# Performance work log

Hardware: AMD Instinct MI355X
Metric: run time of the kernel (lower is better)

Reference implementation:

```python
import jax, jax.numpy as jnp
import numpy as np

D_MODEL = 1024
NUM_HEADS = 16
HEAD_DIM = D_MODEL // NUM_HEADS
B, S = 2, 2048


def setup_inputs() -> dict:
    key = jax.random.key(0)
    ks = jax.random.split(key, 5)
    x = jax.random.normal(ks[0], (B, S, D_MODEL), dtype=jnp.float32)
    # nn.Linear weights are [out_features, in_features]
    Wq = jax.random.normal(ks[1], (D_MODEL, D_MODEL), dtype=jnp.float32) / np.sqrt(D_MODEL)
    Wk = jax.random.normal(ks[2], (HEAD_DIM, D_MODEL), dtype=jnp.float32) / np.sqrt(D_MODEL)
    Wv = jax.random.normal(ks[3], (HEAD_DIM, D_MODEL), dtype=jnp.float32) / np.sqrt(D_MODEL)
    Wo = jax.random.normal(ks[4], (D_MODEL, D_MODEL), dtype=jnp.float32) / np.sqrt(D_MODEL)
    # causal mask, broadcastable to [B, H, S, S]; mask==0 positions get -inf
    mask = jnp.tril(jnp.ones((S, S), dtype=bool))[None, None]
    return {"x": x, "Wq": Wq, "Wk": Wk, "Wv": Wv, "Wo": Wo, "mask": mask}


def reference(x, Wq, Wk, Wv, Wo, mask):
    Bsz, Sl, D = x.shape
    H, hd = NUM_HEADS, HEAD_DIM
    q = (x @ Wq.T).reshape(Bsz, Sl, H, hd)          # [B,S,H,hd]
    k = x @ Wk.T                                    # [B,S,hd] (single shared KV head)
    v = x @ Wv.T                                    # [B,S,hd]
    scale = 1.0 / np.sqrt(hd).astype(np.float32)
    # scores: [B,H,S,S] — full O(n^2) matrix, as in the original module
    scores = jnp.einsum('bshd,btd->bhst', q, k) * scale
    scores = jnp.where(mask, scores, -jnp.inf)
    attn = jax.nn.softmax(scores, axis=-1)
    out = jnp.einsum('bhst,btd->bshd', attn, v).reshape(Bsz, Sl, D)
    return out @ Wo.T
```

## Files before the change

### kernel.cpp

```cpp
#include <hip/hip_runtime.h>
#include <hip/hip_bf16.h>
#include <math.h>

#define BB 2
#define SS 2048
#define DD 1024
#define NH 16
#define HD 64
#define MM (BB * SS)

#define BK 32

typedef __hip_bfloat16 bf16;
typedef __bf16 bf16_t;
typedef __attribute__((ext_vector_type(8))) __bf16 bf16x8;
typedef __attribute__((ext_vector_type(4))) __bf16 bf16x4;
typedef __attribute__((ext_vector_type(4))) float floatx4;

#define SCALEQ 0.18033688011112042f

__global__ void detect_dtype(const unsigned int* __restrict__ x, int* __restrict__ flag) {
    const int tid = threadIdx.x;
    int good = 0;
    for (int i = tid; i < 256; i += 64) {
        unsigned int bits = (x[i] & 0xFFFFu) << 16;
        float v = __uint_as_float(bits);
        float av = fabsf(v);
        if (av == 0.f || (av >= 9.5367431640625e-7f && av <= 64.f)) good++;
    }
#pragma unroll
    for (int s = 1; s < 64; s <<= 1) good += __shfl_xor(good, s);
    if (tid == 0) { flag[0] = (good >= 240) ? 0 : 1; flag[1] = 0; }
}

__device__ __forceinline__ void conv_seg(const void* __restrict__ in,
                                         bf16_t* __restrict__ out,
                                         int n, int f, int tid, int T) {
    if (f) {
        const float* p = (const float*)in;
        for (int i = tid * 8; i < n; i += T * 8) {
            float4 a = *(const float4*)(p + i);
            float4 b = *(const float4*)(p + i + 4);
            bf16x8 o;
            o[0] = (bf16_t)a.x; o[1] = (bf16_t)a.y; o[2] = (bf16_t)a.z; o[3] = (bf16_t)a.w;
            o[4] = (bf16_t)b.x; o[5] = (bf16_t)b.y; o[6] = (bf16_t)b.z; o[7] = (bf16_t)b.w;
            *(bf16x8*)(out + i) = o;
        }
    } else {
        const bf16_t* p = (const bf16_t*)in;
        for (int i = tid * 8; i < n; i += T * 8)
            *(bf16x8*)(out + i) = *(const bf16x8*)(p + i);
    }
}

__global__ __launch_bounds__(256) void conv_all(const void* __restrict__ x,
                                                const void* __restrict__ wq,
                                                const void* __restrict__ wk,
                                                const void* __restrict__ wv,
                                                const void* __restrict__ wo,
                                                bf16_t* __restrict__ xb,
                                                bf16_t* __restrict__ wqb,
                                                bf16_t* __restrict__ wkb,
                                                bf16_t* __restrict__ wvb,
                                                bf16_t* __restrict__ wob,
                                                const int* __restrict__ flag) {
    const int f = *flag;
    const int tid = blockIdx.x * blockDim.x + threadIdx.x;
    const int T = gridDim.x * blockDim.x;
    conv_seg(x, xb, MM * DD, f, tid, T);
    conv_seg(wq, wqb, DD * DD, f, tid, T);
    conv_seg(wk, wkb, HD * DD, f, tid, T);
    conv_seg(wv, wvb, HD * DD, f, tid, T);
    conv_seg(wo, wob, DD * DD, f, tid, T);
}

#define KP 40

__global__ __launch_bounds__(256) void proj_qkv_b(const bf16_t* __restrict__ X,
                                                  const bf16_t* __restrict__ Wq,
                                                  const bf16_t* __restrict__ Wk,
                                                  const bf16_t* __restrict__ Wv,
                                                  bf16_t* __restrict__ QA,
                                                  bf16_t* __restrict__ Kp,
                                                  bf16_t* __restrict__ VpT) {
    __shared__ bf16_t As[64 * KP];
    __shared__ bf16_t Bs[64 * KP];

    const int tid = threadIdx.x;
    const int wave = tid >> 6, lane = tid & 63;
    const int lo = lane & 15, quad = lane >> 4;
    const int wr = wave >> 1, wc = wave & 1;
    const int rowBase = blockIdx.x * 64;
    const int cb = blockIdx.y;

    const int rS = tid >> 2;
    const int c8 = (tid & 3) * 8;

    const bf16_t* arow = X + (size_t)(rowBase + rS) * DD + c8;
    const bf16_t* wrow;
    if (cb < 16)       wrow = Wq + (size_t)(cb * 64 + rS) * DD + c8;
    else if (cb == 16) wrow = Wk + (size_t)rS * DD + c8;
    else               wrow = Wv + (size_t)rS * DD + c8;

    floatx4 acc[2][2];
#pragma unroll
    for (int i = 0; i < 2; i++)
#pragma unroll
        for (int j = 0; j < 2; j++) acc[i][j] = (floatx4){0.f, 0.f, 0.f, 0.f};

    bf16x8 aR0 = *(const bf16x8*)(arow);
    bf16x8 bR0 = *(const bf16x8*)(wrow);
    bf16x8 aR1 = *(const bf16x8*)(arow + BK);
    bf16x8 bR1 = *(const bf16x8*)(wrow + BK);

    for (int k0 = 0; k0 < DD; k0 += 2 * BK) {
        __syncthreads();
        *(bf16x8*)&As[rS * KP + c8] = aR0;
        *(bf16x8*)&Bs[rS * KP + c8] = bR0;
        __syncthreads();
        if (k0 + 2 * BK < DD) {
            aR0 = *(const bf16x8*)(arow + k0 + 2 * BK);
            bR0 = *(const bf16x8*)(wrow + k0 + 2 * BK);
        }
        {
            bf16x8 afr[2], bfr[2];
#pragma unroll
            for (int i = 0; i < 2; i++)
                afr[i] = *(const bf16x8*)&As[(wr * 32 + i * 16 + lo) * KP + quad * 8];
#pragma unroll
            for (int j = 0; j < 2; j++)
                bfr[j] = *(const bf16x8*)&Bs[(wc * 32 + j * 16 + lo) * KP + quad * 8];
#pragma unroll
            for (int i = 0; i < 2; i++)
#pragma unroll
                for (int j = 0; j < 2; j++)
                    acc[i][j] = __builtin_amdgcn_mfma_f32_16x16x32_bf16(afr[i], bfr[j], acc[i][j], 0, 0, 0);
        }
        __syncthreads();
        *(bf16x8*)&As[rS * KP + c8] = aR1;
        *(bf16x8*)&Bs[rS * KP + c8] = bR1;
        __syncthreads();
        if (k0 + 3 * BK < DD) {
            aR1 = *(const bf16x8*)(arow + k0 + 3 * BK);
            bR1 = *(const bf16x8*)(wrow + k0 + 3 * BK);
        }
        {
            bf16x8 afr[2], bfr[2];
#pragma unroll
            for (int i = 0; i < 2; i++)
                afr[i] = *(const bf16x8*)&As[(wr * 32 + i * 16 + lo) * KP + quad * 8];
#pragma unroll
            for (int j = 0; j < 2; j++)
                bfr[j] = *(const bf16x8*)&Bs[(wc * 32 + j * 16 + lo) * KP + quad * 8];
#pragma unroll
            for (int i = 0; i < 2; i++)
#pragma unroll
                for (int j = 0; j < 2; j++)
                    acc[i][j] = __builtin_amdgcn_mfma_f32_16x16x32_bf16(afr[i], bfr[j], acc[i][j], 0, 0, 0);
        }
    }

#pragma unroll
    for (int i = 0; i < 2; i++)
#pragma unroll
        for (int j = 0; j < 2; j++)
#pragma unroll
            for (int reg = 0; reg < 4; reg++) {
                int row = rowBase + wr * 32 + i * 16 + quad * 4 + reg;
                int c = wc * 32 + j * 16 + lo;
                float v = acc[i][j][reg];
                if (cb < 16) {
                    QA[(size_t)row * DD + cb * 64 + c] = (bf16_t)(v * SCALEQ);
                } else if (cb == 16) {
                    Kp[(size_t)row * HD + c] = (bf16_t)v;
                } else {
                    VpT[((size_t)(row >> 11) * HD + c) * SS + (row & (SS - 1))] = (bf16_t)v;
                }
            }
}

__global__ __launch_bounds__(256) void proj_o_b(const bf16_t* __restrict__ AO,
                                                const bf16_t* __restrict__ Wo,
                                                void* __restrict__ Cout,
                                                const int* __restrict__ flagOut) {
    const int fout = *flagOut;

    __shared__ bf16_t As[64 * KP];
    __shared__ bf16_t Bs[64 * KP];

    const int tid = threadIdx.x;
    const int wave = tid >> 6, lane = tid & 63;
    const int lo = lane & 15, quad = lane >> 4;
    const int wr = wave >> 1, wc = wave & 1;
    const int rowBase = blockIdx.x * 64;
    const int colBase = blockIdx.y * 64;

    const int rS = tid >> 2;
    const int c8 = (tid & 3) * 8;

    const bf16_t* arow = AO + (size_t)(rowBase + rS) * DD + c8;
    const bf16_t* wrow = Wo + (size_t)(colBase + rS) * DD + c8;

    floatx4 acc[2][2];
#pragma unroll
    for (int i = 0; i < 2; i++)
#pragma unroll
        for (int j = 0; j < 2; j++) acc[i][j] = (floatx4){0.f, 0.f, 0.f, 0.f};

    bf16x8 aR0 = *(const bf16x8*)(arow);
    bf16x8 bR0 = *(const bf16x8*)(wrow);
    bf16x8 aR1 = *(const bf16x8*)(arow + BK);
    bf16x8 bR1 = *(const bf16x8*)(wrow + BK);

    for (int k0 = 0; k0 < DD; k0 += 2 * BK) {
        __syncthreads();
        *(bf16x8*)&As[rS * KP + c8] = aR0;
        *(bf16x8*)&Bs[rS * KP + c8] = bR0;
        __syncthreads();
        if (k0 + 2 * BK < DD) {
            aR0 = *(const bf16x8*)(arow + k0 + 2 * BK);
            bR0 = *(const bf16x8*)(wrow + k0 + 2 * BK);
        }
        {
            bf16x8 afr[2], bfr[2];
#pragma unroll
            for (int i = 0; i < 2; i++)
                afr[i] = *(const bf16x8*)&As[(wr * 32 + i * 16 + lo) * KP + quad * 8];
#pragma unroll
            for (int j = 0; j < 2; j++)
                bfr[j] = *(const bf16x8*)&Bs[(wc * 32 + j * 16 + lo) * KP + quad * 8];
#pragma unroll
            for (int i = 0; i < 2; i++)
#pragma unroll
                for (int j = 0; j < 2; j++)
                    acc[i][j] = __builtin_amdgcn_mfma_f32_16x16x32_bf16(afr[i], bfr[j], acc[i][j], 0, 0, 0);
        }
        __syncthreads();
        *(bf16x8*)&As[rS * KP + c8] = aR1;
        *(bf16x8*)&Bs[rS * KP + c8] = bR1;
        __syncthreads();
        if (k0 + 3 * BK < DD) {
            aR1 = *(const bf16x8*)(arow + k0 + 3 * BK);
            bR1 = *(const bf16x8*)(wrow + k0 + 3 * BK);
        }
        {
            bf16x8 afr[2], bfr[2];
#pragma unroll
            for (int i = 0; i < 2; i++)
                afr[i] = *(const bf16x8*)&As[(wr * 32 + i * 16 + lo) * KP + quad * 8];
#pragma unroll
            for (int j = 0; j < 2; j++)
                bfr[j] = *(const bf16x8*)&Bs[(wc * 32 + j * 16 + lo) * KP + quad * 8];
#pragma unroll
            for (int i = 0; i < 2; i++)
#pragma unroll
                for (int j = 0; j < 2; j++)
                    acc[i][j] = __builtin_amdgcn_mfma_f32_16x16x32_bf16(afr[i], bfr[j], acc[i][j], 0, 0, 0);
        }
    }

#pragma unroll
    for (int i = 0; i < 2; i++)
#pragma unroll
        for (int j = 0; j < 2; j++)
#pragma unroll
            for (int reg = 0; reg < 4; reg++) {
                int row = rowBase + wr * 32 + i * 16 + quad * 4 + reg;
                int col = colBase + wc * 32 + j * 16 + lo;
                size_t idx = (size_t)row * DD + col;
                if (fout) ((float*)Cout)[idx] = acc[i][j][reg];
                else      ((bf16_t*)Cout)[idx] = (bf16_t)acc[i][j][reg];
            }
}

__device__ __forceinline__ bf16x4 cvt4(float4 v) {
    bf16x4 o;
    o[0] = (bf16_t)v.x; o[1] = (bf16_t)v.y; o[2] = (bf16_t)v.z; o[3] = (bf16_t)v.w;
    return o;
}

__global__ __launch_bounds__(256) void proj_qkv(const void* __restrict__ X,
                                                const void* __restrict__ Wq,
                                                const void* __restrict__ Wk,
                                                const void* __restrict__ Wv,
                                                bf16_t* __restrict__ QA,
                                                bf16_t* __restrict__ Kp,
                                                bf16_t* __restrict__ VpT,
                                                const int* __restrict__ flag) {
    const int f = *flag;

    __shared__ bf16_t As[128 * KP];
    __shared__ bf16_t Ws[64 * KP];

    const int tid = threadIdx.x;
    const int wave = tid >> 6, lane = tid & 63;
    const int lo = lane & 15, quad = lane >> 4;
    const int rb = wave * 32;
    const int cb = blockIdx.x;
    const int rowBase = blockIdx.y * 128;

    floatx4 acc[2][4];
#pragma unroll
    for (int i = 0; i < 2; i++)
#pragma unroll
        for (int j = 0; j < 4; j++) acc[i][j] = (floatx4){0.f, 0.f, 0.f, 0.f};

    if (f) {
        const int rA = tid >> 3, sg = tid & 7;
        const float* arow[4];
        const float* wrow[2];
#pragma unroll
        for (int p = 0; p < 4; p++)
            arow[p] = (const float*)X + (size_t)(rowBase + rA + 32 * p) * DD;
#pragma unroll
        for (int p = 0; p < 2; p++) {
            int row = rA + 32 * p;
            if (cb < 16)       wrow[p] = (const float*)Wq + (size_t)(cb * 64 + row) * DD;
            else if (cb == 16) wrow[p] = (const float*)Wk + (size_t)row * DD;
            else               wrow[p] = (const float*)Wv + (size_t)row * DD;
        }
        float4 aR[4], wR[2];
#pragma unroll
        for (int p = 0; p < 4; p++) aR[p] = *(const float4*)(arow[p] + sg * 4);
#pragma unroll
        for (int p = 0; p < 2; p++) wR[p] = *(const float4*)(wrow[p] + sg * 4);

        for (int k0 = 0; k0 < DD; k0 += BK) {
            __syncthreads();
#pragma unroll
            for (int p = 0; p < 4; p++)
                *(bf16x4*)&As[(rA + 32 * p) * KP + sg * 4] = cvt4(aR[p]);
#pragma unroll
            for (int p = 0; p < 2; p++)
                *(bf16x4*)&Ws[(rA + 32 * p) * KP + sg * 4] = cvt4(wR[p]);
            __syncthreads();
            if (k0 + BK < DD) {
#pragma unroll
                for (int p = 0; p < 4; p++) aR[p] = *(const float4*)(arow[p] + k0 + BK + sg * 4);
#pragma unroll
                for (int p = 0; p < 2; p++) wR[p] = *(const float4*)(wrow[p] + k0 + BK + sg * 4);
            }
            bf16x8 afr[2], bfr[4];
#pragma unroll
            for (int i = 0; i < 2; i++)
                afr[i] = *(const bf16x8*)&As[(rb + i * 16 + lo) * KP + quad * 8];
#pragma unroll
            for (int j = 0; j < 4; j++)
                bfr[j] = *(const bf16x8*)&Ws[(j * 16 + lo) * KP + quad * 8];
#pragma unroll
            for (int i = 0; i < 2; i++)
#pragma unroll
                for (int j = 0; j < 4; j++)
                    acc[i][j] = __builtin_amdgcn_mfma_f32_16x16x32_bf16(afr[i], bfr[j], acc[i][j], 0, 0, 0);
        }
    } else {
        const int rA = tid >> 2, sg = tid & 3;
        const bf16_t* arow[2];
        const bf16_t* wrow;
#pragma unroll
        for (int p = 0; p < 2; p++)
            arow[p] = (const bf16_t*)X + (size_t)(rowBase + rA + 64 * p) * DD;
        if (cb < 16)       wrow = (const bf16_t*)Wq + (size_t)(cb * 64 + rA) * DD;
        else if (cb == 16) wrow = (const bf16_t*)Wk + (size_t)rA * DD;
        else               wrow = (const bf16_t*)Wv + (size_t)rA * DD;
        bf16x8 aR[2], wR;
#pragma unroll
        for (int p = 0; p < 2; p++) aR[p] = *(const bf16x8*)(arow[p] + sg * 8);
        wR = *(const bf16x8*)(wrow + sg * 8);

        for (int k0 = 0; k0 < DD; k0 += BK) {
            __syncthreads();
#pragma unroll
            for (int p = 0; p < 2; p++)
                *(bf16x8*)&As[(rA + 64 * p) * KP + sg * 8] = aR[p];
            *(bf16x8*)&Ws[rA * KP + sg * 8] = wR;
            __syncthreads();
            if (k0 + BK < DD) {
#pragma unroll
                for (int p = 0; p < 2; p++) aR[p] = *(const bf16x8*)(arow[p] + k0 + BK + sg * 8);
                wR = *(const bf16x8*)(wrow + k0 + BK + sg * 8);
            }
            bf16x8 afr[2], bfr[4];
#pragma unroll
            for (int i = 0; i < 2; i++)
                afr[i] = *(const bf16x8*)&As[(rb + i * 16 + lo) * KP + quad * 8];
#pragma unroll
            for (int j = 0; j < 4; j++)
                bfr[j] = *(const bf16x8*)&Ws[(j * 16 + lo) * KP + quad * 8];
#pragma unroll
            for (int i = 0; i < 2; i++)
#pragma unroll
                for (int j = 0; j < 4; j++)
                    acc[i][j] = __builtin_amdgcn_mfma_f32_16x16x32_bf16(afr[i], bfr[j], acc[i][j], 0, 0, 0);
        }
    }

#pragma unroll
    for (int i = 0; i < 2; i++)
#pragma unroll
        for (int j = 0; j < 4; j++)
#pragma unroll
            for (int reg = 0; reg < 4; reg++) {
                int row = rowBase + rb + i * 16 + quad * 4 + reg;
                int col = j * 16 + lo;
                if (cb < 16) {
                    QA[(size_t)row * DD + cb * 64 + col] = (bf16_t)(acc[i][j][reg] * SCALEQ);
                } else if (cb == 16) {
                    Kp[(size_t)row * HD + col] = (bf16_t)acc[i][j][reg];
                } else {
                    VpT[((size_t)(row >> 11) * HD + col) * SS + (row & (SS - 1))] =
                        (bf16_t)acc[i][j][reg];
                }
            }
}

__global__ __launch_bounds__(256) void proj_o(const bf16_t* __restrict__ AO,
                                              const void* __restrict__ Wo,
                                              void* __restrict__ Cout,
                                              const int* __restrict__ flagW,
                                              const int* __restrict__ flagOut) {
    const int f = *flagW;
    const int fout = *flagOut;

    __shared__ bf16_t As[128 * KP];
    __shared__ bf16_t Ws[64 * KP];

    const int tid = threadIdx.x;
    const int wave = tid >> 6, lane = tid & 63;
    const int lo = lane & 15, quad = lane >> 4;
    const int rb = wave * 32;
    const int colBase = blockIdx.x * 64;
    const int rowBase = blockIdx.y * 128;

    floatx4 acc[2][4];
#pragma unroll
    for (int i = 0; i < 2; i++)
#pragma unroll
        for (int j = 0; j < 4; j++) acc[i][j] = (floatx4){0.f, 0.f, 0.f, 0.f};

    const int rA2 = tid >> 2, sgA = tid & 3;
    const bf16_t* arow[2] = {AO + (size_t)(rowBase + rA2) * DD,
                             AO + (size_t)(rowBase + rA2 + 64) * DD};
    bf16x8 aR[2];
#pragma unroll
    for (int p = 0; p < 2; p++) aR[p] = *(const bf16x8*)(arow[p] + sgA * 8);

    if (f) {
        const int rW = tid >> 3, sgW = tid & 7;
        const float* wrow[2];
#pragma unroll
        for (int p = 0; p < 2; p++)
            wrow[p] = (const float*)Wo + (size_t)(colBase + rW + 32 * p) * DD;
        float4 wR[2];
#pragma unroll
        for (int p = 0; p < 2; p++) wR[p] = *(const float4*)(wrow[p] + sgW * 4);

        for (int k0 = 0; k0 < DD; k0 += BK) {
            __syncthreads();
#pragma unroll
            for (int p = 0; p < 2; p++)
                *(bf16x8*)&As[(rA2 + 64 * p) * KP + sgA * 8] = aR[p];
#pragma unroll
            for (int p = 0; p < 2; p++)
                *(bf16x4*)&Ws[(rW + 32 * p) * KP + sgW * 4] = cvt4(wR[p]);
            __syncthreads();
            if (k0 + BK < DD) {
#pragma unroll
                for (int p = 0; p < 2; p++) aR[p] = *(const bf16x8*)(arow[p] + k0 + BK + sgA * 8);
#pragma unroll
                for (int p = 0; p < 2; p++) wR[p] = *(const float4*)(wrow[p] + k0 + BK + sgW * 4);
            }
            bf16x8 afr[2], bfr[4];
#pragma unroll
            for (int i = 0; i < 2; i++)
                afr[i] = *(const bf16x8*)&As[(rb + i * 16 + lo) * KP + quad * 8];
#pragma unroll
            for (int j = 0; j < 4; j++)
                bfr[j] = *(const bf16x8*)&Ws[(j * 16 + lo) * KP + quad * 8];
#pragma unroll
            for (int i = 0; i < 2; i++)
#pragma unroll
                for (int j = 0; j < 4; j++)
                    acc[i][j] = __builtin_amdgcn_mfma_f32_16x16x32_bf16(afr[i], bfr[j], acc[i][j], 0, 0, 0);
        }
    } else {
        const bf16_t* wrow = (const bf16_t*)Wo + (size_t)(colBase + rA2) * DD;
        bf16x8 wR = *(const bf16x8*)(wrow + sgA * 8);

        for (int k0 = 0; k0 < DD; k0 += BK) {
            __syncthreads();
#pragma unroll
            for (int p = 0; p < 2; p++)
                *(bf16x8*)&As[(rA2 + 64 * p) * KP + sgA * 8] = aR[p];
            *(bf16x8*)&Ws[rA2 * KP + sgA * 8] = wR;
            __syncthreads();
            if (k0 + BK < DD) {
#pragma unroll
                for (int p = 0; p < 2; p++) aR[p] = *(const bf16x8*)(arow[p] + k0 + BK + sgA * 8);
                wR = *(const bf16x8*)(wrow + k0 + BK + sgA * 8);
            }
            bf16x8 afr[2], bfr[4];
#pragma unroll
            for (int i = 0; i < 2; i++)
                afr[i] = *(const bf16x8*)&As[(rb + i * 16 + lo) * KP + quad * 8];
#pragma unroll
            for (int j = 0; j < 4; j++)
                bfr[j] = *(const bf16x8*)&Ws[(j * 16 + lo) * KP + quad * 8];
#pragma unroll
            for (int i = 0; i < 2; i++)
#pragma unroll
                for (int j = 0; j < 4; j++)
                    acc[i][j] = __builtin_amdgcn_mfma_f32_16x16x32_bf16(afr[i], bfr[j], acc[i][j], 0, 0, 0);
        }
    }

#pragma unroll
    for (int i = 0; i < 2; i++)
#pragma unroll
        for (int j = 0; j < 4; j++)
#pragma unroll
            for (int reg = 0; reg < 4; reg++) {
                int row = rowBase + rb + i * 16 + quad * 4 + reg;
                int col = colBase + j * 16 + lo;
                size_t idx = (size_t)row * DD + col;
                if (fout) ((float*)Cout)[idx] = acc[i][j][reg];
                else      ((bf16_t*)Cout)[idx] = (bf16_t)acc[i][j][reg];
            }
}

#define PSTR 40
#define DMTHR 8.0f

__global__ __launch_bounds__(512, 4) void attn_mfma(const bf16_t* Q,
                                                    const bf16_t* __restrict__ K,
                                                    const bf16_t* __restrict__ Vt,
                                                    bf16_t* O) {
    const int h = blockIdx.y, b = blockIdx.z;
    const int tid = threadIdx.x;
    const int wq = tid >> 6, lane = tid & 63;
    const int lo = lane & 15, quad = lane >> 4;
    const int x = blockIdx.x;

    const int nA = x + 1;
    int na = 1, bestc = 0x7fffffff;
#pragma unroll
    for (int a = 1; a <= 7; ++a) {
        int cA = (nA + a - 1) / a;
        int cB = (65 - nA + (7 - a)) / (8 - a);
        int c = cA > cB ? cA : cB;
        if (c < bestc) { bestc = c; na = a; }
    }
    int qt, pos, gs;
    if (wq < na) { qt = x;      pos = wq;      gs = na; }
    else         { qt = 63 - x; pos = wq - na; gs = 8 - na; }
    const int q0 = qt * 32;
    const int n = qt + 1;
    const int itS = (n * pos) / gs;
    const int itE = (n * (pos + 1)) / gs;

    __shared__ __align__(16) char smem[4 * 32 * 64 * 4];
    __shared__ float MrgML[4][2][2][16];
    bf16_t* Pw = (bf16_t*)smem + wq * (32 * PSTR);
    float (*MrgO)[32 * 64] = (float (*)[32 * 64])smem;

    bf16x8 qf[2][2];
#pragma unroll
    for (int s = 0; s < 2; s++)
#pragma unroll
        for (int hf = 0; hf < 2; hf++)
            qf[s][hf] = *(const bf16x8*)(Q + ((size_t)(b * SS + q0 + s * 16 + lo)) * DD +
                                         h * HD + hf * 32 + quad * 8);

    floatx4 Oacc[2][4];
    float m_i[2], l_ln[2];
#pragma unroll
    for (int s = 0; s < 2; s++) {
#pragma unroll
        for (int dt = 0; dt < 4; dt++) Oacc[s][dt] = (floatx4){0.f, 0.f, 0.f, 0.f};
        m_i[s] = -1e30f; l_ln[s] = 0.f;
    }

    const bf16_t* Kb = K + (size_t)b * SS * HD;
    const bf16_t* Vb = Vt + (size_t)b * HD * SS;

    if (itS < itE) {
        bf16x8 kf[2][2];
#pragma unroll
        for (int kt = 0; kt < 2; kt++)
#pragma unroll
            for (int hf = 0; hf < 2; hf++)
                kf[kt][hf] = *(const bf16x8*)(Kb + (size_t)(itS * 32 + kt * 16 + lo) * HD +
                                              hf * 32 + quad * 8);

        for (int it = itS; it < itE; it++) {
            const int t0 = it * 32;

            bf16x8 vf[4];
#pragma unroll
            for (int dt = 0; dt < 4; dt++)
                vf[dt] = *(const bf16x8*)(Vb + (size_t)(dt * 16 + lo) * SS + t0 + quad * 8);

            bf16x8 kn[2][2];
            if (it + 1 < itE) {
#pragma unroll
                for (int kt = 0; kt < 2; kt++)
#pragma unroll
                    for (int hf = 0; hf < 2; hf++)
                        kn[kt][hf] = *(const bf16x8*)(Kb + (size_t)(t0 + 32 + kt * 16 + lo) * HD +
                                                      hf * 32 + quad * 8);
            }

            floatx4 st[2][2];
#pragma unroll
            for (int s = 0; s < 2; s++)
#pragma unroll
                for (int kt = 0; kt < 2; kt++) {
                    floatx4 z = (floatx4){0.f, 0.f, 0.f, 0.f};
                    z = __builtin_amdgcn_mfma_f32_16x16x32_bf16(kf[kt][0], qf[s][0], z, 0, 0, 0);
                    z = __builtin_amdgcn_mfma_f32_16x16x32_bf16(kf[kt][1], qf[s][1], z, 0, 0, 0);
                    st[s][kt] = z;
                }

            if (it == qt) {
#pragma unroll
                for (int s = 0; s < 2; s++) {
                    int q = q0 + s * 16 + lo;
#pragma unroll
                    for (int kt = 0; kt < 2; kt++)
#pragma unroll
                        for (int reg = 0; reg < 4; reg++)
                            if (t0 + kt * 16 + quad * 4 + reg > q) st[s][kt][reg] = -1e30f;
                }
            }

#pragma unroll
            for (int s = 0; s < 2; s++) {
                float lm = fmaxf(fmaxf(fmaxf(st[s][0][0], st[s][0][1]), fmaxf(st[s][0][2], st[s][0][3])),
                                 fmaxf(fmaxf(st[s][1][0], st[s][1][1]), fmaxf(st[s][1][2], st[s][1][3])));
                if (__any(lm > m_i[s] + DMTHR)) {
                    float mx = fmaxf(lm, __shfl_xor(lm, 16));
                    mx = fmaxf(mx, __shfl_xor(mx, 32));
                    float mn = fmaxf(m_i[s], mx);
                    float al = exp2f(m_i[s] - mn);
                    m_i[s] = mn;
                    l_ln[s] *= al;
#pragma unroll
                    for (int dt = 0; dt < 4; dt++) Oacc[s][dt] *= al;
                }
                float p[2][4];
#pragma unroll
                for (int kt = 0; kt < 2; kt++)
#pragma unroll
                    for (int reg = 0; reg < 4; reg++)
                        p[kt][reg] = exp2f(st[s][kt][reg] - m_i[s]);
                l_ln[s] += ((p[0][0] + p[0][1]) + (p[0][2] + p[0][3])) +
                           ((p[1][0] + p[1][1]) + (p[1][2] + p[1][3]));
#pragma unroll
                for (int kt = 0; kt < 2; kt++) {
                    bf16x4 pk;
#pragma unroll
                    for (int reg = 0; reg < 4; reg++) pk[reg] = (bf16_t)p[kt][reg];
                    *(bf16x4*)&Pw[(s * 16 + lo) * PSTR + kt * 16 + quad * 4] = pk;
                }
            }

            asm volatile("s_waitcnt lgkmcnt(0)" ::: "memory");

            bf16x8 pb[2];
#pragma unroll
            for (int s = 0; s < 2; s++)
                pb[s] = *(const bf16x8*)&Pw[(s * 16 + lo) * PSTR + quad * 8];
#pragma unroll
            for (int s = 0; s < 2; s++)
#pragma unroll
                for (int dt = 0; dt < 4; dt++)
                    Oacc[s][dt] = __builtin_amdgcn_mfma_f32_16x16x32_bf16(vf[dt], pb[s], Oacc[s][dt], 0, 0, 0);

#pragma unroll
            for (int kt = 0; kt < 2; kt++)
#pragma unroll
                for (int hf = 0; hf < 2; hf++) kf[kt][hf] = kn[kt][hf];
        }
    }

    float l_i[2];
#pragma unroll
    for (int s = 0; s < 2; s++) {
        float l = l_ln[s];
        l += __shfl_xor(l, 16);
        l += __shfl_xor(l, 32);
        l_i[s] = l;
    }

    for (int step = 1; step < 8; step <<= 1) {
        const bool pub = (pos & (2 * step - 1)) == step;
        const bool cmb = ((pos & (2 * step - 1)) == 0) && (pos + step < gs);
        __syncthreads();
        if (pub) {
            float* Ob = MrgO[wq >> 1];
#pragma unroll
            for (int s = 0; s < 2; s++) {
#pragma unroll
                for (int dt = 0; dt < 4; dt++)
#pragma unroll
                    for (int reg = 0; reg < 4; reg++)
                        Ob[(s * 16 + dt * 4 + reg) * 64 + lane] = Oacc[s][dt][reg];
                if (quad == 0) {
                    MrgML[wq >> 1][s][0][lo] = m_i[s];
                    MrgML[wq >> 1][s][1][lo] = l_i[s];
                }
            }
        }
        __syncthreads();
        if (cmb) {
            const int bu = (wq + step) >> 1;
            const float* Ob = MrgO[bu];
#pragma unroll
            for (int s = 0; s < 2; s++) {
                float m1 = MrgML[bu][s][0][lo];
                float l1 = MrgML[bu][s][1][lo];
                float mm = fmaxf(m_i[s], m1);
                float a0 = exp2f(m_i[s] - mm);
                float a1 = exp2f(m1 - mm);
                m_i[s] = mm;
                l_i[s] = l_i[s] * a0 + l1 * a1;
#pragma unroll
                for (int dt = 0; dt < 4; dt++)
#pragma unroll
                    for (int reg = 0; reg < 4; reg++)
                        Oacc[s][dt][reg] = Oacc[s][dt][reg] * a0 +
                                           Ob[(s * 16 + dt * 4 + reg) * 64 + lane] * a1;
            }
        }
    }

    if (pos == 0) {
#pragma unroll
        for (int s = 0; s < 2; s++) {
            float linv = 1.f / l_i[s];
            bf16_t* Orow = O + ((size_t)(b * SS + q0 + s * 16 + lo)) * DD + h * HD;
#pragma unroll
            for (int dt = 0; dt < 4; dt++) {
                bf16x4 ov;
#pragma unroll
                for (int reg = 0; reg < 4; reg++)
                    ov[reg] = (bf16_t)(Oacc[s][dt][reg] * linv);
                *(bf16x4*)&Orow[dt * 16 + quad * 4] = ov;
            }
        }
    }
}

extern "C" void kernel_launch(void* const* d_in, const int* in_sizes, int n_in,
                              void* d_out, int out_size, void* d_ws, size_t ws_size,
                              hipStream_t stream) {
    const void* x  = d_in[0];
    const void* Wq = d_in[1];
    const void* Wk = d_in[2];
    const void* Wv = d_in[3];
    const void* Wo = d_in[4];

    char* ws = (char*)d_ws;
    int* flag = (int*)ws;
    bf16_t* QA  = (bf16_t*)(ws + 256);
    bf16_t* Kp  = QA + (size_t)MM * DD;
    bf16_t* VpT = Kp + (size_t)MM * HD;
    bf16_t* Xb  = VpT + (size_t)BB * HD * SS;
    bf16_t* Wqb = Xb + (size_t)MM * DD;
    bf16_t* Wkb = Wqb + (size_t)DD * DD;
    bf16_t* Wvb = Wkb + (size_t)HD * DD;
    bf16_t* Wob = Wvb + (size_t)HD * DD;
    size_t need = (size_t)((char*)(Wob + (size_t)DD * DD) - ws);

    detect_dtype<<<1, 64, 0, stream>>>((const unsigned int*)x, flag);

    if (ws_size >= need) {
        conv_all<<<dim3(1024), dim3(256), 0, stream>>>(x, Wq, Wk, Wv, Wo,
                                                       Xb, Wqb, Wkb, Wvb, Wob, flag);
        proj_qkv_b<<<dim3(MM / 64, 18), dim3(256), 0, stream>>>(Xb, Wqb, Wkb, Wvb,
                                                                QA, Kp, VpT);
        attn_mfma<<<dim3(32, NH, BB), dim3(512), 0, stream>>>(QA, Kp, VpT, QA);
        proj_o_b<<<dim3(MM / 64, 16), dim3(256), 0, stream>>>(QA, Wob, d_out, flag);
    } else {
        proj_qkv<<<dim3(18, MM / 128), dim3(256), 0, stream>>>(x, Wq, Wk, Wv,
                                                               QA, Kp, VpT, flag);
        attn_mfma<<<dim3(32, NH, BB), dim3(512), 0, stream>>>(QA, Kp, VpT, QA);
        proj_o<<<dim3(16, MM / 128), dim3(256), 0, stream>>>(QA, Wo, d_out,
                                                             flag, flag);
    }
}
```

Baseline: 209.9 us.

## Split attention into one-tile-per-block with 4 waves; simplify fallback projection GEMMs

The attention kernel drops the paired-tile scheme, where each 512-thread block split a short and a long query tile across 8 waves with a balanced split. It now uses 256-thread blocks, one query tile each, with the KV range split evenly over 4 waves, and launches 64 blocks per head in reverse order. Launch bounds change to allow 5 blocks per CU. The fallback projection kernels, used only when the workspace is too small, are rewritten as simpler 64x64 tiles without register prefetch. Blocks now do uneven amounts of work, so load balance depends on the scheduler issuing the long tiles first.

```diff
diff --git a/kernel.cpp b/kernel.cpp
--- a/kernel.cpp
+++ b/kernel.cpp
@@ -273,255 +273,148 @@
             }
 }
 
-__device__ __forceinline__ bf16x4 cvt4(float4 v) {
-    bf16x4 o;
-    o[0] = (bf16_t)v.x; o[1] = (bf16_t)v.y; o[2] = (bf16_t)v.z; o[3] = (bf16_t)v.w;
-    return o;
-}
-
-__global__ __launch_bounds__(256) void proj_qkv(const void* __restrict__ X,
-                                                const void* __restrict__ Wq,
-                                                const void* __restrict__ Wk,
-                                                const void* __restrict__ Wv,
-                                                bf16_t* __restrict__ QA,
-                                                bf16_t* __restrict__ Kp,
-                                                bf16_t* __restrict__ VpT,
-                                                const int* __restrict__ flag) {
+__device__ __forceinline__ bf16x8 ld8(const void* p, int f, size_t idx) {
+    if (f) {
+        const float* q = (const float*)p + idx;
+        float4 a = *(const float4*)(q);
+        float4 b = *(const float4*)(q + 4);
+        bf16x8 o;
+        o[0] = (bf16_t)a.x; o[1] = (bf16_t)a.y; o[2] = (bf16_t)a.z; o[3] = (bf16_t)a.w;
+        o[4] = (bf16_t)b.x; o[5] = (bf16_t)b.y; o[6] = (bf16_t)b.z; o[7] = (bf16_t)b.w;
+        return o;
+    }
+    return *(const bf16x8*)((const bf16_t*)p + idx);
+}
+
+__global__ __launch_bounds__(256) void proj_qkv_f(const void* __restrict__ X,
+                                                  const void* __restrict__ Wq,
+                                                  const void* __restrict__ Wk,
+                                                  const void* __restrict__ Wv,
+                                                  bf16_t* __restrict__ QA,
+                                                  bf16_t* __restrict__ Kp,
+                                                  bf16_t* __restrict__ VpT,
+                                                  const int* __restrict__ flag) {
     const int f = *flag;
-
-    __shared__ bf16_t As[128 * KP];
-    __shared__ bf16_t Ws[64 * KP];
+    __shared__ bf16_t As[64 * KP];
+    __shared__ bf16_t Bs[64 * KP];
 
     const int tid = threadIdx.x;
     const int wave = tid >> 6, lane = tid & 63;
     const int lo = lane & 15, quad = lane >> 4;
-    const int rb = wave * 32;
-    const int cb = blockIdx.x;
-    const int rowBase = blockIdx.y * 128;
-
-    floatx4 acc[2][4];
-#pragma unroll
-    for (int i = 0; i < 2; i++)
-#pragma unroll
-        for (int j = 0; j < 4; j++) acc[i][j] = (floatx4){0.f, 0.f, 0.f, 0.f};
-
-    if (f) {
-        const int rA = tid >> 3, sg = tid & 7;
-        const float* arow[4];
-        const float* wrow[2];
-#pragma unroll
-        for (int p = 0; p < 4; p++)
-            arow[p] = (const float*)X + (size_t)(rowBase + rA + 32 * p) * DD;
-#pragma unroll
-        for (int p = 0; p < 2; p++) {
-            int row = rA + 32 * p;
-            if (cb < 16)       wrow[p] = (const float*)Wq + (size_t)(cb * 64 + row) * DD;
-            else if (cb == 16) wrow[p] = (const float*)Wk + (size_t)row * DD;
-            else               wrow[p] = (const float*)Wv + (size_t)row * DD;
-        }
-        float4 aR[4], wR[2];
-#pragma unroll
-        for (int p = 0; p < 4; p++) aR[p] = *(const float4*)(arow[p] + sg * 4);
-#pragma unroll
-        for (int p = 0; p < 2; p++) wR[p] = *(const float4*)(wrow[p] + sg * 4);
-
-        for (int k0 = 0; k0 < DD; k0 += BK) {
-            __syncthreads();
-#pragma unroll
-            for (int p = 0; p < 4; p++)
-                *(bf16x4*)&As[(rA + 32 * p) * KP + sg * 4] = cvt4(aR[p]);
-#pragma unroll
-            for (int p = 0; p < 2; p++)
-                *(bf16x4*)&Ws[(rA + 32 * p) * KP + sg * 4] = cvt4(wR[p]);
-            __syncthreads();
-            if (k0 + BK < DD) {
-#pragma unroll
-                for (int p = 0; p < 4; p++) aR[p] = *(const float4*)(arow[p] + k0 + BK + sg * 4);
-#pragma unroll
-                for (int p = 0; p < 2; p++) wR[p] = *(const float4*)(wrow[p] + k0 + BK + sg * 4);
-            }
-            bf16x8 afr[2], bfr[4];
-#pragma unroll
-            for (int i = 0; i < 2; i++)
-                afr[i] = *(const bf16x8*)&As[(rb + i * 16 + lo) * KP + quad * 8];
-#pragma unroll
-            for (int j = 0; j < 4; j++)
-                bfr[j] = *(const bf16x8*)&Ws[(j * 16 + lo) * KP + quad * 8];
-#pragma unroll
-            for (int i = 0; i < 2; i++)
-#pragma unroll
-                for (int j = 0; j < 4; j++)
-                    acc[i][j] = __builtin_amdgcn_mfma_f32_16x16x32_bf16(afr[i], bfr[j], acc[i][j], 0, 0, 0);
-        }
-    } else {
-        const int rA = tid >> 2, sg = tid & 3;
-        const bf16_t* arow[2];
-        const bf16_t* wrow;
-#pragma unroll
-        for (int p = 0; p < 2; p++)
-            arow[p] = (const bf16_t*)X + (size_t)(rowBase + rA + 64 * p) * DD;
-        if (cb < 16)       wrow = (const bf16_t*)Wq + (size_t)(cb * 64 + rA) * DD;
-        else if (cb == 16) wrow = (const bf16_t*)Wk + (size_t)rA * DD;
-        else               wrow = (const bf16_t*)Wv + (size_t)rA * DD;
-        bf16x8 aR[2], wR;
-#pragma unroll
-        for (int p = 0; p < 2; p++) aR[p] = *(const bf16x8*)(arow[p] + sg * 8);
-        wR = *(const bf16x8*)(wrow + sg * 8);
-
-        for (int k0 = 0; k0 < DD; k0 += BK) {
-            __syncthreads();
-#pragma unroll
-            for (int p = 0; p < 2; p++)
-                *(bf16x8*)&As[(rA + 64 * p) * KP + sg * 8] = aR[p];
-            *(bf16x8*)&Ws[rA * KP + sg * 8] = wR;
-            __syncthreads();
-            if (k0 + BK < DD) {
-#pragma unroll
-                for (int p = 0; p < 2; p++) aR[p] = *(const bf16x8*)(arow[p] + k0 + BK + sg * 8);
-                wR = *(const bf16x8*)(wrow + k0 + BK + sg * 8);
-            }
-            bf16x8 afr[2], bfr[4];
-#pragma unroll
-            for (int i = 0; i < 2; i++)
-                afr[i] = *(const bf16x8*)&As[(rb + i * 16 + lo) * KP + quad * 8];
-#pragma unroll
-            for (int j = 0; j < 4; j++)
-                bfr[j] = *(const bf16x8*)&Ws[(j * 16 + lo) * KP + quad * 8];
-#pragma unroll
-            for (int i = 0; i < 2; i++)
-#pragma unroll
-                for (int j = 0; j < 4; j++)
-                    acc[i][j] = __builtin_amdgcn_mfma_f32_16x16x32_bf16(afr[i], bfr[j], acc[i][j], 0, 0, 0);
-        }
-    }
-
-#pragma unroll
-    for (int i = 0; i < 2; i++)
-#pragma unroll
-        for (int j = 0; j < 4; j++)
+    const int wr = wave >> 1, wc = wave & 1;
+    const int rowBase = blockIdx.x * 64;
+    const int cb = blockIdx.y;
+
+    const int rS = tid >> 2;
+    const int c8 = (tid & 3) * 8;
+
+    size_t aidx = (size_t)(rowBase + rS) * DD + c8;
+    size_t widx;
+    const void* Wsrc;
+    if (cb < 16)       { Wsrc = Wq; widx = (size_t)(cb * 64 + rS) * DD + c8; }
+    else if (cb == 16) { Wsrc = Wk; widx = (size_t)rS * DD + c8; }
+    else               { Wsrc = Wv; widx = (size_t)rS * DD + c8; }
+
+    floatx4 acc[2][2];
+#pragma unroll
+    for (int i = 0; i < 2; i++)
+#pragma unroll
+        for (int j = 0; j < 2; j++) acc[i][j] = (floatx4){0.f, 0.f, 0.f, 0.f};
+
+    for (int k0 = 0; k0 < DD; k0 += BK) {
+        __syncthreads();
+        *(bf16x8*)&As[rS * KP + c8] = ld8(X, f, aidx + k0);
+        *(bf16x8*)&Bs[rS * KP + c8] = ld8(Wsrc, f, widx + k0);
+        __syncthreads();
+        bf16x8 afr[2], bfr[2];
+#pragma unroll
+        for (int i = 0; i < 2; i++)
+            afr[i] = *(const bf16x8*)&As[(wr * 32 + i * 16 + lo) * KP + quad * 8];
+#pragma unroll
+        for (int j = 0; j < 2; j++)
+            bfr[j] = *(const bf16x8*)&Bs[(wc * 32 + j * 16 + lo) * KP + quad * 8];
+#pragma unroll
+        for (int i = 0; i < 2; i++)
+#pragma unroll
+            for (int j = 0; j < 2; j++)
+                acc[i][j] = __builtin_amdgcn_mfma_f32_16x16x32_bf16(afr[i], bfr[j], acc[i][j], 0, 0, 0);
+    }
+
+#pragma unroll
+    for (int i = 0; i < 2; i++)
+#pragma unroll
+        for (int j = 0; j < 2; j++)
 #pragma unroll
             for (int reg = 0; reg < 4; reg++) {
-                int row = rowBase + rb + i * 16 + quad * 4 + reg;
-                int col = j * 16 + lo;
+                int row = rowBase + wr * 32 + i * 16 + quad * 4 + reg;
+                int c = wc * 32 + j * 16 + lo;
+                float v = acc[i][j][reg];
                 if (cb < 16) {
-                    QA[(size_t)row * DD + cb * 64 + col] = (bf16_t)(acc[i][j][reg] * SCALEQ);
+                    QA[(size_t)row * DD + cb * 64 + c] = (bf16_t)(v * SCALEQ);
                 } else if (cb == 16) {
-                    Kp[(size_t)row * HD + col] = (bf16_t)acc[i][j][reg];
+                    Kp[(size_t)row * HD + c] = (bf16_t)v;
                 } else {
-                    VpT[((size_t)(row >> 11) * HD + col) * SS + (row & (SS - 1))] =
-                        (bf16_t)acc[i][j][reg];
+                    VpT[((size_t)(row >> 11) * HD + c) * SS + (row & (SS - 1))] = (bf16_t)v;
                 }
             }
 }
 
-__global__ __launch_bounds__(256) void proj_o(const bf16_t* __restrict__ AO,
-                                              const void* __restrict__ Wo,
-                                              void* __restrict__ Cout,
-                                              const int* __restrict__ flagW,
-                                              const int* __restrict__ flagOut) {
+__global__ __launch_bounds__(256) void proj_o_f(const bf16_t* __restrict__ AO,
+                                                const void* __restrict__ Wo,
+                                                void* __restrict__ Cout,
+                                                const int* __restrict__ flagW,
+                                                const int* __restrict__ flagOut) {
     const int f = *flagW;
     const int fout = *flagOut;
-
-    __shared__ bf16_t As[128 * KP];
-    __shared__ bf16_t Ws[64 * KP];
+    __shared__ bf16_t As[64 * KP];
+    __shared__ bf16_t Bs[64 * KP];
 
     const int tid = threadIdx.x;
     const int wave = tid >> 6, lane = tid & 63;
     const int lo = lane & 15, quad = lane >> 4;
-    const int rb = wave * 32;
-    const int colBase = blockIdx.x * 64;
-    const int rowBase = blockIdx.y * 128;
-
-    floatx4 acc[2][4];
-#pragma unroll
-    for (int i = 0; i < 2; i++)
-#pragma unroll
-        for (int j = 0; j < 4; j++) acc[i][j] = (floatx4){0.f, 0.f, 0.f, 0.f};
-
-    const int rA2 = tid >> 2, sgA = tid & 3;
-    const bf16_t* arow[2] = {AO + (size_t)(rowBase + rA2) * DD,
-                             AO + (size_t)(rowBase + rA2 + 64) * DD};
-    bf16x8 aR[2];
-#pragma unroll
-    for (int p = 0; p < 2; p++) aR[p] = *(const bf16x8*)(arow[p] + sgA * 8);
-
-    if (f) {
-        const int rW = tid >> 3, sgW = tid & 7;
-        const float* wrow[2];
-#pragma unroll
-        for (int p = 0; p < 2; p++)
-            wrow[p] = (const float*)Wo + (size_t)(colBase + rW + 32 * p) * DD;
-        float4 wR[2];
-#pragma unroll
-        for (int p = 0; p < 2; p++) wR[p] = *(const float4*)(wrow[p] + sgW * 4);
-
-        for (int k0 = 0; k0 < DD; k0 += BK) {
-            __syncthreads();
-#pragma unroll
-            for (int p = 0; p < 2; p++)
-                *(bf16x8*)&As[(rA2 + 64 * p) * KP + sgA * 8] = aR[p];
-#pragma unroll
-            for (int p = 0; p < 2; p++)
-                *(bf16x4*)&Ws[(rW + 32 * p) * KP + sgW * 4] = cvt4(wR[p]);
-            __syncthreads();
-            if (k0 + BK < DD) {
-#pragma unroll
-                for (int p = 0; p < 2; p++) aR[p] = *(const bf16x8*)(arow[p] + k0 + BK + sgA * 8);
-#pragma unroll
-                for (int p = 0; p < 2; p++) wR[p] = *(const float4*)(wrow[p] + k0 + BK + sgW * 4);
-            }
-            bf16x8 afr[2], bfr[4];
-#pragma unroll
-            for (int i = 0; i < 2; i++)
-                afr[i] = *(const bf16x8*)&As[(rb + i * 16 + lo) * KP + quad * 8];
-#pragma unroll
-            for (int j = 0; j < 4; j++)
-                bfr[j] = *(const bf16x8*)&Ws[(j * 16 + lo) * KP + quad * 8];
-#pragma unroll
-            for (int i = 0; i < 2; i++)
-#pragma unroll
-                for (int j = 0; j < 4; j++)
-                    acc[i][j] = __builtin_amdgcn_mfma_f32_16x16x32_bf16(afr[i], bfr[j], acc[i][j], 0, 0, 0);
-        }
-    } else {
-        const bf16_t* wrow = (const bf16_t*)Wo + (size_t)(colBase + rA2) * DD;
-        bf16x8 wR = *(const bf16x8*)(wrow + sgA * 8);
-
-        for (int k0 = 0; k0 < DD; k0 += BK) {
-            __syncthreads();
-#pragma unroll
-            for (int p = 0; p < 2; p++)
-                *(bf16x8*)&As[(rA2 + 64 * p) * KP + sgA * 8] = aR[p];
-            *(bf16x8*)&Ws[rA2 * KP + sgA * 8] = wR;
-            __syncthreads();
-            if (k0 + BK < DD) {
-#pragma unroll
-                for (int p = 0; p < 2; p++) aR[p] = *(const bf16x8*)(arow[p] + k0 + BK + sgA * 8);
-                wR = *(const bf16x8*)(wrow + k0 + BK + sgA * 8);
-            }
-            bf16x8 afr[2], bfr[4];
-#pragma unroll
-            for (int i = 0; i < 2; i++)
-                afr[i] = *(const bf16x8*)&As[(rb + i * 16 + lo) * KP + quad * 8];
-#pragma unroll
-            for (int j = 0; j < 4; j++)
-                bfr[j] = *(const bf16x8*)&Ws[(j * 16 + lo) * KP + quad * 8];
-#pragma unroll
-            for (int i = 0; i < 2; i++)
-#pragma unroll
-                for (int j = 0; j < 4; j++)
-                    acc[i][j] = __builtin_amdgcn_mfma_f32_16x16x32_bf16(afr[i], bfr[j], acc[i][j], 0, 0, 0);
-        }
-    }
-
-#pragma unroll
-    for (int i = 0; i < 2; i++)
-#pragma unroll
-        for (int j = 0; j < 4; j++)
+    const int wr = wave >> 1, wc = wave & 1;
+    const int rowBase = blockIdx.x * 64;
+    const int colBase = blockIdx.y * 64;
+
+    const int rS = tid >> 2;
+    const int c8 = (tid & 3) * 8;
+
+    size_t aidx = (size_t)(rowBase + rS) * DD + c8;
+    size_t widx = (size_t)(colBase + rS) * DD + c8;
+
+    floatx4 acc[2][2];
+#pragma unroll
+    for (int i = 0; i < 2; i++)
+#pragma unroll
+        for (int j = 0; j < 2; j++) acc[i][j] = (floatx4){0.f, 0.f, 0.f, 0.f};
+
+    for (int k0 = 0; k0 < DD; k0 += BK) {
+        __syncthreads();
+        *(bf16x8*)&As[rS * KP + c8] = *(const bf16x8*)(AO + aidx + k0);
+        *(bf16x8*)&Bs[rS * KP + c8] = ld8(Wo, f, widx + k0);
+        __syncthreads();
+        bf16x8 afr[2], bfr[2];
+#pragma unroll
+        for (int i = 0; i < 2; i++)
+            afr[i] = *(const bf16x8*)&As[(wr * 32 + i * 16 + lo) * KP + quad * 8];
+#pragma unroll
+        for (int j = 0; j < 2; j++)
+            bfr[j] = *(const bf16x8*)&Bs[(wc * 32 + j * 16 + lo) * KP + quad * 8];
+#pragma unroll
+        for (int i = 0; i < 2; i++)
+#pragma unroll
+            for (int j = 0; j < 2; j++)
+                acc[i][j] = __builtin_amdgcn_mfma_f32_16x16x32_bf16(afr[i], bfr[j], acc[i][j], 0, 0, 0);
+    }
+
+#pragma unroll
+    for (int i = 0; i < 2; i++)
+#pragma unroll
+        for (int j = 0; j < 2; j++)
 #pragma unroll
             for (int reg = 0; reg < 4; reg++) {
-                int row = rowBase + rb + i * 16 + quad * 4 + reg;
-                int col = colBase + j * 16 + lo;
+                int row = rowBase + wr * 32 + i * 16 + quad * 4 + reg;
+                int col = colBase + wc * 32 + j * 16 + lo;
                 size_t idx = (size_t)row * DD + col;
                 if (fout) ((float*)Cout)[idx] = acc[i][j][reg];
                 else      ((bf16_t*)Cout)[idx] = (bf16_t)acc[i][j][reg];
@@ -531,7 +424,7 @@
 #define PSTR 40
 #define DMTHR 8.0f
 
-__global__ __launch_bounds__(512, 4) void attn_mfma(const bf16_t* Q,
+__global__ __launch_bounds__(256, 5) void attn_mfma(const bf16_t* Q,
                                                     const bf16_t* __restrict__ K,
                                                     const bf16_t* __restrict__ Vt,
                                                     bf16_t* O) {
@@ -539,27 +432,14 @@
     const int tid = threadIdx.x;
     const int wq = tid >> 6, lane = tid & 63;
     const int lo = lane & 15, quad = lane >> 4;
-    const int x = blockIdx.x;
-
-    const int nA = x + 1;
-    int na = 1, bestc = 0x7fffffff;
-#pragma unroll
-    for (int a = 1; a <= 7; ++a) {
-        int cA = (nA + a - 1) / a;
-        int cB = (65 - nA + (7 - a)) / (8 - a);
-        int c = cA > cB ? cA : cB;
-        if (c < bestc) { bestc = c; na = a; }
-    }
-    int qt, pos, gs;
-    if (wq < na) { qt = x;      pos = wq;      gs = na; }
-    else         { qt = 63 - x; pos = wq - na; gs = 8 - na; }
+    const int qt = 63 - blockIdx.x;
     const int q0 = qt * 32;
     const int n = qt + 1;
-    const int itS = (n * pos) / gs;
-    const int itE = (n * (pos + 1)) / gs;
-
-    __shared__ __align__(16) char smem[4 * 32 * 64 * 4];
-    __shared__ float MrgML[4][2][2][16];
+    const int itS = (n * wq) >> 2;
+    const int itE = (n * (wq + 1)) >> 2;
+
+    __shared__ __align__(16) char smem[2 * 32 * 64 * 4];
+    __shared__ float MrgML[2][2][2][16];
     bf16_t* Pw = (bf16_t*)smem + wq * (32 * PSTR);
     float (*MrgO)[32 * 64] = (float (*)[32 * 64])smem;
 
@@ -692,9 +572,9 @@
         l_i[s] = l;
     }
 
-    for (int step = 1; step < 8; step <<= 1) {
-        const bool pub = (pos & (2 * step - 1)) == step;
-        const bool cmb = ((pos & (2 * step - 1)) == 0) && (pos + step < gs);
+    for (int step = 1; step < 4; step <<= 1) {
+        const bool pub = (wq & (2 * step - 1)) == step;
+        const bool cmb = ((wq & (2 * step - 1)) == 0) && (wq + step < 4);
         __syncthreads();
         if (pub) {
             float* Ob = MrgO[wq >> 1];
@@ -734,7 +614,7 @@
         }
     }
 
-    if (pos == 0) {
+    if (wq == 0) {
 #pragma unroll
         for (int s = 0; s < 2; s++) {
             float linv = 1.f / l_i[s];
@@ -779,13 +659,13 @@
                                                        Xb, Wqb, Wkb, Wvb, Wob, flag);
         proj_qkv_b<<<dim3(MM / 64, 18), dim3(256), 0, stream>>>(Xb, Wqb, Wkb, Wvb,
                                                                 QA, Kp, VpT);
-        attn_mfma<<<dim3(32, NH, BB), dim3(512), 0, stream>>>(QA, Kp, VpT, QA);
+        attn_mfma<<<dim3(64, NH, BB), dim3(256), 0, stream>>>(QA, Kp, VpT, QA);
         proj_o_b<<<dim3(MM / 64, 16), dim3(256), 0, stream>>>(QA, Wob, d_out, flag);
     } else {
-        proj_qkv<<<dim3(18, MM / 128), dim3(256), 0, stream>>>(x, Wq, Wk, Wv,
-                                                               QA, Kp, VpT, flag);
-        attn_mfma<<<dim3(32, NH, BB), dim3(512), 0, stream>>>(QA, Kp, VpT, QA);
-        proj_o<<<dim3(16, MM / 128), dim3(256), 0, stream>>>(QA, Wo, d_out,
-                                                             flag, flag);
-    }
-}
+        proj_qkv_f<<<dim3(MM / 64, 18), dim3(256), 0, stream>>>(x, Wq, Wk, Wv,
+                                                                QA, Kp, VpT, flag);
+        attn_mfma<<<dim3(64, NH, BB), dim3(256), 0, stream>>>(QA, Kp, VpT, QA);
+        proj_o_f<<<dim3(MM / 64, 16), dim3(256), 0, stream>>>(QA, Wo, d_out,
+                                                              flag, flag);
+    }
+}
```

After: 366.4 us. +74.6%, slower.
